# Kernel optimization log

Measured on AMD Instinct MI355X. Metric: run time of the kernel, lower is better.

The kernel has to match this reference:

```python
import jax, jax.numpy as jnp
import numpy as np
import math

# ---- static config (matches init_kwargs) ----
MUL = 16                       # multiplicity of 0e and 1o irreps in/out
IN_DIM = 4 * MUL               # 16x0e + 16x1o -> 16 + 48 = 64 channels
DIAMETER = 7.0
RADIUS = DIAMETER / 2.0
NRB = 8                        # num_radial_basis
STEPS = (1.0, 1.0, 1.0)
N_PATHS = 5                    # 0x0->0, 1x1->0, 0x1->1, 1x0->1, 1x1->1
WEIGHT_NUMEL = N_PATHS * MUL * MUL  # 1280


def _lattice():
    axes = []
    for st in STEPS:
        s = math.floor(RADIUS / st)
        axes.append(np.arange(-s, s + 1.0) * st)
    return np.stack(np.meshgrid(*axes, indexing='ij'), axis=-1).astype(np.float32)  # [kx,ky,kz,3]


def _radial_emb(r):
    # e3nn soft_one_hot_linspace, basis='smooth_finite', cutoff=True
    values = np.linspace(0.0, RADIUS, NRB + 2)[1:-1].astype(np.float32)
    step = values[1] - values[0]
    diff = (r[..., None] - values) / step
    def u(t):  # soft unit step: exp(-1/t) for t>0 else 0
        return np.where(t > 0.0, np.exp(-1.0 / np.where(t > 0.0, t, 1.0)), 0.0)
    return (1.14136 * math.e ** 2 * u(diff + 1.0) * u(1.0 - diff)).astype(np.float32)


def _spherical_harmonics(lat):
    # normalize=True, normalization='component': Y0 = 1, Y1 = sqrt(3) * unit_vec
    n = np.linalg.norm(lat, axis=-1, keepdims=True)
    unit = np.where(n > 0, lat / np.where(n > 0, n, 1.0), 0.0)
    return np.ones(lat.shape[:-1], np.float32), (math.sqrt(3.0) * unit).astype(np.float32)


_LAT = _lattice()
_EMB = jnp.asarray(_radial_emb(np.linalg.norm(_LAT, axis=-1)))  # [kx,ky,kz,NRB]
_sh0_np, _sh1_np = _spherical_harmonics(_LAT)
_SH0, _SH1 = jnp.asarray(_sh0_np), jnp.asarray(_sh1_np)
_eps_np = np.zeros((3, 3, 3), np.float32)
for _i, _j, _k in [(0, 1, 2), (1, 2, 0), (2, 0, 1)]:
    _eps_np[_i, _j, _k] = 1.0
    _eps_np[_i, _k, _j] = -1.0
_EPS = jnp.asarray(_eps_np)


def _build_kernel(tp_weight):
    """Radial-basis matmul + CG tensor-product -> conv kernel [out,in,kx,ky,kz]."""
    kx, ky, kz = _LAT.shape[:3]
    nk = kx * ky * kz
    w = jnp.einsum('xyzb,bn->xyzn', _EMB, tp_weight) / nk
    w = w.reshape(kx, ky, kz, N_PATHS, MUL, MUL)
    w1, w2, w3, w4, w5 = [w[..., p, :, :] for p in range(N_PATHS)]
    # e3nn path weights ('component' norm, 'element' path norm): sqrt(dim_out / fan_in)
    a0 = math.sqrt(1.0 / (2 * MUL))  # -> 0e: paths 1,2 each mul1*mul2 = MUL
    a1 = math.sqrt(3.0 / (3 * MUL))  # -> 1o: paths 3,4,5
    c1 = a0                          # w3j(0,0,0) = 1
    c2 = a0 / math.sqrt(3.0)         # w3j(1,1,0) = delta/sqrt(3)
    c3 = a1 / math.sqrt(3.0)         # w3j(0,1,1) = delta/sqrt(3)
    c4 = a1 / math.sqrt(3.0)         # w3j(1,0,1) = delta/sqrt(3)
    c5 = a1 / math.sqrt(6.0)         # w3j(1,1,1) = eps/sqrt(6)
    Kss = c1 * _SH0[..., None, None] * w1                                  # [k,u,o]
    Kvs = c2 * jnp.einsum('xyzi,xyzuo->xyzuio', _SH1, w2)                  # [k,u,3,o]
    Ksv = c3 * jnp.einsum('xyzk,xyzuo->xyzuok', _SH1, w3)                  # [k,u,o,3]
    eye3 = jnp.eye(3, dtype=w.dtype)
    Kvv = (c4 * jnp.einsum('xyz,ik,xyzuo->xyzuiok', _SH0, eye3, w4)
           + c5 * jnp.einsum('ijk,xyzj,xyzuo->xyzuiok', _EPS, _SH1, w5))   # [k,u,3,o,3]
    top = jnp.concatenate([Kss, Ksv.reshape(kx, ky, kz, MUL, 3 * MUL)], axis=-1)
    bot = jnp.concatenate([Kvs.reshape(kx, ky, kz, 3 * MUL, MUL),
                           Kvv.reshape(kx, ky, kz, 3 * MUL, 3 * MUL)], axis=-1)
    K = jnp.concatenate([top, bot], axis=-2)                               # [kx,ky,kz,in,out]
    return jnp.transpose(K, (4, 3, 0, 1, 2))                               # oixyz


def setup_inputs() -> dict:
    key = jax.random.key(0)
    k1, k2, k3, k4 = jax.random.split(key, 4)
    x = jax.random.normal(k1, (2, IN_DIM, 40, 40, 40), jnp.float32)
    sc_w0 = jax.random.normal(k2, (MUL, MUL), jnp.float32)
    sc_w1 = jax.random.normal(k3, (MUL, MUL), jnp.float32)
    tp_weight = jax.random.normal(k4, (NRB, WEIGHT_NUMEL), jnp.float32)
    return {"x": x, "sc_w0": sc_w0, "sc_w1": sc_w1, "tp_weight": tp_weight}


def reference(x, sc_w0, sc_w1, tp_weight):
    B = x.shape[0]
    sp = x.shape[2:]
    inv = 1.0 / math.sqrt(MUL)  # e3nn Linear fan-in normalization
    x0 = x[:, :MUL]                                  # [B,MUL,D,H,W]
    x1 = x[:, MUL:].reshape(B, MUL, 3, *sp)          # [B,MUL,3,D,H,W]
    sc0 = jnp.einsum('uo,budhw->bodhw', sc_w0, x0) * inv
    sc1 = jnp.einsum('uo,buidhw->boidhw', sc_w1, x1) * inv
    sc = jnp.concatenate([sc0, sc1.reshape(B, 3 * MUL, *sp)], axis=1)
    K = _build_kernel(tp_weight)
    pad = [(s // 2, s // 2) for s in K.shape[2:]]
    conv = jax.lax.conv_general_dilated(
        x, K, window_strides=(1, 1, 1), padding=pad,
        dimension_numbers=('NCDHW', 'OIDHW', 'NCDHW'))
    return sc + conv
```

## Files before the change

kernel.cpp:

```cpp
#include <hip/hip_runtime.h>
#include <stdint.h>


#define NT_REAL 179
#define NT_PAD  180
#define NGRP    45

#define XCH  1557376
#define XCHB ((size_t)XCH * 2)

typedef short s16x8 __attribute__((ext_vector_type(8)));
typedef float f32x4 __attribute__((ext_vector_type(4)));

struct Taps {
  int n;
  short dl16[NT_PAD];
  unsigned char dz[NT_PAD], dy[NT_PAD], dx[NT_PAD];
};
constexpr Taps mk_taps() {
  Taps t{};
  t.n = 0;
  for (int a = 0; a < 7; ++a)
    for (int b = 0; b < 7; ++b)
      for (int c = 0; c < 7; ++c) {
        int d2 = (a-3)*(a-3) + (b-3)*(b-3) + (c-3)*(c-3);
        if (d2 <= 12) {
          t.dz[t.n] = (unsigned char)a; t.dy[t.n] = (unsigned char)b;
          t.dx[t.n] = (unsigned char)c;
          t.dl16[t.n] = (short)((a*14 + b)*16 + c);
          ++t.n;
        }
      }
  for (int i = t.n; i < NT_PAD; ++i) {
    t.dz[i] = 3; t.dy[i] = 3; t.dx[i] = 3; t.dl16[i] = t.dl16[0];
  }
  return t;
}
__device__ constexpr Taps TAPS = mk_taps();
static_assert(mk_taps().n == NT_REAL, "tap count");

struct DL4s { unsigned long long v[NGRP]; };
constexpr DL4s mk_dl4() {
  DL4s d{};
  Taps t = mk_taps();
  for (int g = 0; g < NGRP; ++g) {
    unsigned long long v = 0;
    for (int q = 0; q < 4; ++q)
      v |= (unsigned long long)(unsigned short)t.dl16[g * 4 + q] << (16 * q);
    d.v[g] = v;
  }
  return d;
}
__device__ constexpr DL4s DL4 = mk_dl4();

static __device__ inline unsigned short f2bf(float f) {
  unsigned int u = __float_as_uint(f);
  unsigned int r = u + 0x7FFFu + ((u >> 16) & 1u);
  return (unsigned short)(r >> 16);
}

__device__ __forceinline__ void gl_lds16(const void* g, void* s) {
  __builtin_amdgcn_global_load_lds(
      (const __attribute__((address_space(1))) void*)g,
      (__attribute__((address_space(3))) void*)s, 16, 0, 0);
}

__global__ void prep(const float* __restrict__ x, const float* __restrict__ scw0,
                     const float* __restrict__ scw1, const float* __restrict__ tpw,
                     unsigned short* __restrict__ Xp, unsigned short* __restrict__ Bwp) {
  __shared__ float buf[160 * 65];
  int tid = threadIdx.x;

  if (blockIdx.x < 800) {
    int blk = blockIdx.x;
    int ys = blk % 10; int t2 = blk / 10; int iz = t2 % 40; int b = t2 / 40;
    int y0 = ys * 4;
    const float* src = x + (size_t)b * 4096000 + (size_t)iz * 1600 + (size_t)y0 * 40;
    for (int e = tid; e < 64 * 160; e += 256) {
      int ch = e / 160, i = e - ch * 160;
      buf[i * 65 + ch] = src[(size_t)ch * 64000 + i];
    }
    __syncthreads();
    for (int f = tid; f < 160 * 8; f += 256) {
      int i = f >> 3, g = f & 7;
      int yy = i / 40, xx = i - yy * 40;
      s16x8 v;
      #pragma unroll
      for (int j = 0; j < 8; ++j) v[j] = (short)f2bf(buf[i * 65 + g * 8 + j]);
      size_t pos = ((size_t)((b * 46 + iz + 3) * 46 + (y0 + yy + 3)) * 46 + (xx + 3));
      *reinterpret_cast<s16x8*>(Xp + (size_t)g * XCH + pos * 8) = v;
    }
    return;
  }

  int t = blockIdx.x - 800;
  float (*wsm)[16][16] = reinterpret_cast<float (*)[16][16]>(buf);

  int dz = TAPS.dz[t], dy = TAPS.dy[t], dx = TAPS.dx[t];
  float fz = dz - 3.0f, fy = dy - 3.0f, fx = dx - 3.0f;
  float d2 = fz*fz + fy*fy + fx*fx;
  float r = sqrtf(d2);

  const float step = 3.5f / 9.0f;
  const float Cc = 1.14136f * 7.38905609893065f;
  float emb[8];
  for (int bb = 0; bb < 8; ++bb) {
    float diff = (r - step * (bb + 1)) / step;
    float t1 = diff + 1.0f, t2 = 1.0f - diff;
    float u1 = (t1 > 0.0f) ? expf(-1.0f / t1) : 0.0f;
    float u2 = (t2 > 0.0f) ? expf(-1.0f / t2) : 0.0f;
    emb[bb] = Cc * u1 * u2;
  }

  int u = tid >> 4, o = tid & 15;
  for (int p = 0; p < 5; ++p) {
    float acc = 0.0f;
    int nidx = (p * 16 + u) * 16 + o;
    for (int bb = 0; bb < 8; ++bb) acc += emb[bb] * tpw[bb * 1280 + nidx];
    wsm[p][u][o] = acc * (1.0f / 343.0f);
  }
  __syncthreads();

  float invr = (d2 > 0.0f) ? (1.7320508075688772f / r) : 0.0f;
  float sh[3] = { fz * invr, fy * invr, fx * invr };

  bool center = (dz == 3 && dy == 3 && dx == 3);
  bool padt = (t >= NT_REAL);
  const float c1 = 0.17677669529663687f;
  const float c2 = 0.10206207261596575f;
  const float c3 = 0.14433756729740643f;
  const float c4 = 0.14433756729740643f;
  const float c5 = 0.10206207261596575f;
  const float inv = 0.25f;

  for (int e = tid; e < 4096; e += 256) {
    int ich = e & 63, och = e >> 6;
    float v = 0.0f;
    if (!padt) {
      if (och < 16) {
        if (ich < 16) {
          v = c1 * wsm[0][ich][och];
          if (center) v += inv * scw0[ich * 16 + och];
        } else {
          int qq = ich - 16; int uu = qq / 3, ii = qq % 3;
          v = c2 * sh[ii] * wsm[1][uu][och];
        }
      } else {
        int qo = och - 16; int oo = qo / 3, kk = qo % 3;
        if (ich < 16) {
          v = c3 * sh[kk] * wsm[2][ich][oo];
        } else {
          int qi = ich - 16; int uu = qi / 3, ii = qi % 3;
          if (ii == kk) {
            v = c4 * wsm[3][uu][oo];
            if (center) v += inv * scw1[uu * 16 + oo];
          } else {
            int jj = 3 - ii - kk;
            float sgn = (((kk - ii + 3) % 3) == 2) ? 1.0f : -1.0f;
            v = c5 * sgn * sh[jj] * wsm[4][uu][oo];
          }
        }
      }
    }
    int chunk = ich >> 3, j = ich & 7, q = t & 3, grp = t >> 2;
    int nt = och >> 4, n = och & 15;
    size_t idx = (((((size_t)chunk * NGRP + grp) * 4 + nt) * 4 + q) * 16 + n) * 8 + j;
    Bwp[idx] = f2bf(v);
  }
}

__global__ __launch_bounds__(256, 2) void conv3d(
    const unsigned short* __restrict__ Xp,
    const unsigned short* __restrict__ Bwp,
    float* __restrict__ out) {
  __shared__ __align__(16) unsigned char smem[76800];
  unsigned char* XH = smem;
  unsigned char* BB = smem + 35840;

  int blk = blockIdx.x;
  int p = ((blk & 7) << 6) | (blk >> 3);
  if (p >= 500) return;
  int b = p / 250; int rem = p - b * 250;
  int tz = rem / 25, ty = (rem / 5) % 5, tx = rem % 5;

  int tid = threadIdx.x;
  int lane = tid & 63;
  int w = tid >> 6;
  int q = lane >> 4, n = lane & 15;
  int qs = q << 4;

  size_t hbase = (size_t)(((b * 46 + tz * 4) * 46 + ty * 8) * 46 + tx * 8) * 16;

  int abase = w * 224 + ((n >> 3) << 4) + (n & 7);

  f32x4 acc[4][4];
  #pragma unroll
  for (int a = 0; a < 4; ++a)
    #pragma unroll
    for (int nt = 0; nt < 4; ++nt) acc[a][nt] = f32x4{0.f, 0.f, 0.f, 0.f};

  auto stageB = [&](int c, int s, unsigned char* dst) {
    const unsigned char* bg = (const unsigned char*)Bwp
        + ((size_t)c * NGRP + s * 5) * 4096;
    for (int k = w; k < 20; k += 4)
      gl_lds16(bg + (k << 10) + lane * 16, dst + (k << 10));
  };
  auto stageH = [&](int c) {
    const unsigned char* xc = (const unsigned char*)Xp + (size_t)c * XCHB + hbase;
    for (int k = w; k < 35; k += 4) {
      int sl = (k << 6) + lane;
      int hx = sl & 15; hx = hx > 13 ? 13 : hx;
      int r = sl >> 4;
      int hz = (r * 2341) >> 15;
      int hy = r - hz * 14;
      gl_lds16(xc + ((size_t)((hz * 46 + hy) * 46 + hx)) * 16, XH + (k << 10));
    }
  };

  stageB(0, 0, BB);

  int t = 0;
  for (int c = 0; c < 8; ++c) {
    stageH(c);
    __syncthreads();
    for (int s = 0; s < 9; ++s, ++t) {
      if (t + 1 < 72) {
        int cn = (s == 8) ? c + 1 : c;
        int sn = (s == 8) ? 0 : s + 1;
        stageB(cn, sn, BB + ((t + 1) & 1) * 20480);
      }
      const unsigned char* BSc = BB + (t & 1) * 20480 + (size_t)lane * 16;
      #pragma unroll
      for (int gg = 0; gg < 5; ++gg) {
        unsigned long long dlv = DL4.v[s * 5 + gg];
        int dl = (int)((dlv >> qs) & 0xFFFFull);
        const unsigned char* ab = XH + ((size_t)(abase + dl) << 4);
        s16x8 a0 = *(const s16x8*)(ab);
        s16x8 a1 = *(const s16x8*)(ab + 512);
        s16x8 a2 = *(const s16x8*)(ab + 1024);
        s16x8 a3 = *(const s16x8*)(ab + 1536);
        const unsigned char* bp = BSc + (gg << 12);
        s16x8 b0 = *(const s16x8*)(bp);
        s16x8 b1 = *(const s16x8*)(bp + 1024);
        s16x8 b2 = *(const s16x8*)(bp + 2048);
        s16x8 b3 = *(const s16x8*)(bp + 3072);
        acc[0][0] = __builtin_amdgcn_mfma_f32_16x16x32_bf16(a0, b0, acc[0][0], 0, 0, 0);
        acc[0][1] = __builtin_amdgcn_mfma_f32_16x16x32_bf16(a0, b1, acc[0][1], 0, 0, 0);
        acc[0][2] = __builtin_amdgcn_mfma_f32_16x16x32_bf16(a0, b2, acc[0][2], 0, 0, 0);
        acc[0][3] = __builtin_amdgcn_mfma_f32_16x16x32_bf16(a0, b3, acc[0][3], 0, 0, 0);
        acc[1][0] = __builtin_amdgcn_mfma_f32_16x16x32_bf16(a1, b0, acc[1][0], 0, 0, 0);
        acc[1][1] = __builtin_amdgcn_mfma_f32_16x16x32_bf16(a1, b1, acc[1][1], 0, 0, 0);
        acc[1][2] = __builtin_amdgcn_mfma_f32_16x16x32_bf16(a1, b2, acc[1][2], 0, 0, 0);
        acc[1][3] = __builtin_amdgcn_mfma_f32_16x16x32_bf16(a1, b3, acc[1][3], 0, 0, 0);
        acc[2][0] = __builtin_amdgcn_mfma_f32_16x16x32_bf16(a2, b0, acc[2][0], 0, 0, 0);
        acc[2][1] = __builtin_amdgcn_mfma_f32_16x16x32_bf16(a2, b1, acc[2][1], 0, 0, 0);
        acc[2][2] = __builtin_amdgcn_mfma_f32_16x16x32_bf16(a2, b2, acc[2][2], 0, 0, 0);
        acc[2][3] = __builtin_amdgcn_mfma_f32_16x16x32_bf16(a2, b3, acc[2][3], 0, 0, 0);
        acc[3][0] = __builtin_amdgcn_mfma_f32_16x16x32_bf16(a3, b0, acc[3][0], 0, 0, 0);
        acc[3][1] = __builtin_amdgcn_mfma_f32_16x16x32_bf16(a3, b1, acc[3][1], 0, 0, 0);
        acc[3][2] = __builtin_amdgcn_mfma_f32_16x16x32_bf16(a3, b2, acc[3][2], 0, 0, 0);
        acc[3][3] = __builtin_amdgcn_mfma_f32_16x16x32_bf16(a3, b3, acc[3][3], 0, 0, 0);
      }
      __syncthreads();
    }
  }

  #pragma unroll
  for (int nt = 0; nt < 4; ++nt) {
    size_t cb = (size_t)(b * 64 + nt * 16 + n) * 64000
              + (size_t)(tz * 4 + w) * 1600
              + (size_t)(tx * 8 + (q & 1) * 4);
    #pragma unroll
    for (int a = 0; a < 4; ++a) {
      float* dst = out + cb + (size_t)(ty * 8 + a * 2 + (q >> 1)) * 40;
      *reinterpret_cast<f32x4*>(dst) = acc[a][nt];
    }
  }
}

extern "C" void kernel_launch(void* const* d_in, const int* in_sizes, int n_in,
                              void* d_out, int out_size, void* d_ws, size_t ws_size,
                              hipStream_t stream) {
  const float* x    = (const float*)d_in[0];
  const float* scw0 = (const float*)d_in[1];
  const float* scw1 = (const float*)d_in[2];
  const float* tpw  = (const float*)d_in[3];
  float* out = (float*)d_out;

  unsigned short* Xp  = (unsigned short*)d_ws;
  unsigned short* Bwp = Xp + (size_t)8 * XCH;

  hipMemsetAsync(Xp, 0, (size_t)8 * XCH * 2, stream);
  prep<<<800 + NT_PAD, 256, 0, stream>>>(x, scw0, scw1, tpw, Xp, Bwp);
  conv3d<<<512, 256, 0, stream>>>(Xp, Bwp, out);
}
```

Baseline: 236.3 us.

## Load weights directly to registers and double-buffer input halo in LDS

Weight (B) fragments are no longer staged through shared memory. Each wave now reads them straight from global memory into registers, with a three-deep software pipeline of register buffers. The input halo tile is double-buffered in LDS, and the next channel chunk is prefetched gradually during the middle groups of the current chunk's compute. This cuts the barriers from one per tap-group step to one per channel chunk. In exchange, every wave fetches B redundantly from global/L2, register pressure rises, and global load latency is now exposed inside the MFMA loop.

```diff
diff --git a/kernel.cpp b/kernel.cpp
--- a/kernel.cpp
+++ b/kernel.cpp
@@ -173,9 +173,7 @@
     const unsigned short* __restrict__ Xp,
     const unsigned short* __restrict__ Bwp,
     float* __restrict__ out) {
-  __shared__ __align__(16) unsigned char smem[76800];
-  unsigned char* XH = smem;
-  unsigned char* BB = smem + 35840;
+  __shared__ __align__(16) unsigned char smem[71680];
 
   int blk = blockIdx.x;
   int p = ((blk & 7) << 6) | (blk >> 3);
@@ -199,70 +197,76 @@
     #pragma unroll
     for (int nt = 0; nt < 4; ++nt) acc[a][nt] = f32x4{0.f, 0.f, 0.f, 0.f};
 
-  auto stageB = [&](int c, int s, unsigned char* dst) {
-    const unsigned char* bg = (const unsigned char*)Bwp
-        + ((size_t)c * NGRP + s * 5) * 4096;
-    for (int k = w; k < 20; k += 4)
-      gl_lds16(bg + (k << 10) + lane * 16, dst + (k << 10));
+  auto stageH1 = [&](int c, unsigned char* dst, int k) {
+    const unsigned char* xc = (const unsigned char*)Xp + (size_t)c * XCHB + hbase;
+    int sl = (k << 6) + lane;
+    int hx = sl & 15; hx = hx > 13 ? 13 : hx;
+    int r = sl >> 4;
+    int hz = (r * 2341) >> 15;
+    int hy = r - hz * 14;
+    gl_lds16(xc + ((size_t)((hz * 46 + hy) * 46 + hx)) * 16, dst + (k << 10));
   };
-  auto stageH = [&](int c) {
-    const unsigned char* xc = (const unsigned char*)Xp + (size_t)c * XCHB + hbase;
-    for (int k = w; k < 35; k += 4) {
-      int sl = (k << 6) + lane;
-      int hx = sl & 15; hx = hx > 13 ? 13 : hx;
-      int r = sl >> 4;
-      int hz = (r * 2341) >> 15;
-      int hy = r - hz * 14;
-      gl_lds16(xc + ((size_t)((hz * 46 + hy) * 46 + hx)) * 16, XH + (k << 10));
-    }
-  };
-
-  stageB(0, 0, BB);
-
-  int t = 0;
+
+  for (int k = w; k < 35; k += 4) stageH1(0, smem, k);
+  __syncthreads();
+
   for (int c = 0; c < 8; ++c) {
-    stageH(c);
+    const unsigned char* XHc = smem + (c & 1) * 35840;
+    unsigned char* XHn = smem + ((c + 1) & 1) * 35840;
+
+    const unsigned char* bgc = (const unsigned char*)Bwp
+        + (size_t)c * (NGRP * 4096) + (size_t)lane * 16;
+
+    s16x8 bf0[4], bf1[4], bf2[4];
+    auto loadB = [&](s16x8* dst, int g) {
+      const s16x8* pp = (const s16x8*)(bgc + (size_t)g * 4096);
+      dst[0] = pp[0]; dst[1] = pp[64]; dst[2] = pp[128]; dst[3] = pp[192];
+    };
+    auto compute = [&](int g, const s16x8* bfr) {
+      unsigned long long dlv = DL4.v[g];
+      int dl = (int)((dlv >> qs) & 0xFFFFull);
+      const unsigned char* ab = XHc + ((size_t)(abase + dl) << 4);
+      s16x8 a0 = *(const s16x8*)(ab);
+      s16x8 a1 = *(const s16x8*)(ab + 512);
+      s16x8 a2 = *(const s16x8*)(ab + 1024);
+      s16x8 a3 = *(const s16x8*)(ab + 1536);
+      acc[0][0] = __builtin_amdgcn_mfma_f32_16x16x32_bf16(a0, bfr[0], acc[0][0], 0, 0, 0);
+      acc[0][1] = __builtin_amdgcn_mfma_f32_16x16x32_bf16(a0, bfr[1], acc[0][1], 0, 0, 0);
+      acc[0][2] = __builtin_amdgcn_mfma_f32_16x16x32_bf16(a0, bfr[2], acc[0][2], 0, 0, 0);
+      acc[0][3] = __builtin_amdgcn_mfma_f32_16x16x32_bf16(a0, bfr[3], acc[0][3], 0, 0, 0);
+      acc[1][0] = __builtin_amdgcn_mfma_f32_16x16x32_bf16(a1, bfr[0], acc[1][0], 0, 0, 0);
+      acc[1][1] = __builtin_amdgcn_mfma_f32_16x16x32_bf16(a1, bfr[1], acc[1][1], 0, 0, 0);
+      acc[1][2] = __builtin_amdgcn_mfma_f32_16x16x32_bf16(a1, bfr[2], acc[1][2], 0, 0, 0);
+      acc[1][3] = __builtin_amdgcn_mfma_f32_16x16x32_bf16(a1, bfr[3], acc[1][3], 0, 0, 0);
+      acc[2][0] = __builtin_amdgcn_mfma_f32_16x16x32_bf16(a2, bfr[0], acc[2][0], 0, 0, 0);
+      acc[2][1] = __builtin_amdgcn_mfma_f32_16x16x32_bf16(a2, bfr[1], acc[2][1], 0, 0, 0);
+      acc[2][2] = __builtin_amdgcn_mfma_f32_16x16x32_bf16(a2, bfr[2], acc[2][2], 0, 0, 0);
+      acc[2][3] = __builtin_amdgcn_mfma_f32_16x16x32_bf16(a2, bfr[3], acc[2][3], 0, 0, 0);
+      acc[3][0] = __builtin_amdgcn_mfma_f32_16x16x32_bf16(a3, bfr[0], acc[3][0], 0, 0, 0);
+      acc[3][1] = __builtin_amdgcn_mfma_f32_16x16x32_bf16(a3, bfr[1], acc[3][1], 0, 0, 0);
+      acc[3][2] = __builtin_amdgcn_mfma_f32_16x16x32_bf16(a3, bfr[2], acc[3][2], 0, 0, 0);
+      acc[3][3] = __builtin_amdgcn_mfma_f32_16x16x32_bf16(a3, bfr[3], acc[3][3], 0, 0, 0);
+    };
+
+    loadB(bf0, 0);
+    loadB(bf1, 1);
+    #pragma unroll 1
+    for (int g = 0; g < NGRP; g += 3) {
+      if (c < 7 && g >= 12 && g <= 36) {
+        int k = ((g - 12) / 3) * 4 + w;
+        if (k < 35) stageH1(c + 1, XHn, k);
+      }
+      int g2 = g + 2 < NGRP ? g + 2 : NGRP - 1;
+      int g3 = g + 3 < NGRP ? g + 3 : NGRP - 1;
+      int g4 = g + 4 < NGRP ? g + 4 : NGRP - 1;
+      loadB(bf2, g2);
+      compute(g, bf0);
+      loadB(bf0, g3);
+      compute(g + 1, bf1);
+      loadB(bf1, g4);
+      compute(g + 2, bf2);
+    }
     __syncthreads();
-    for (int s = 0; s < 9; ++s, ++t) {
-      if (t + 1 < 72) {
-        int cn = (s == 8) ? c + 1 : c;
-        int sn = (s == 8) ? 0 : s + 1;
-        stageB(cn, sn, BB + ((t + 1) & 1) * 20480);
-      }
-      const unsigned char* BSc = BB + (t & 1) * 20480 + (size_t)lane * 16;
-      #pragma unroll
-      for (int gg = 0; gg < 5; ++gg) {
-        unsigned long long dlv = DL4.v[s * 5 + gg];
-        int dl = (int)((dlv >> qs) & 0xFFFFull);
-        const unsigned char* ab = XH + ((size_t)(abase + dl) << 4);
-        s16x8 a0 = *(const s16x8*)(ab);
-        s16x8 a1 = *(const s16x8*)(ab + 512);
-        s16x8 a2 = *(const s16x8*)(ab + 1024);
-        s16x8 a3 = *(const s16x8*)(ab + 1536);
-        const unsigned char* bp = BSc + (gg << 12);
-        s16x8 b0 = *(const s16x8*)(bp);
-        s16x8 b1 = *(const s16x8*)(bp + 1024);
-        s16x8 b2 = *(const s16x8*)(bp + 2048);
-        s16x8 b3 = *(const s16x8*)(bp + 3072);
-        acc[0][0] = __builtin_amdgcn_mfma_f32_16x16x32_bf16(a0, b0, acc[0][0], 0, 0, 0);
-        acc[0][1] = __builtin_amdgcn_mfma_f32_16x16x32_bf16(a0, b1, acc[0][1], 0, 0, 0);
-        acc[0][2] = __builtin_amdgcn_mfma_f32_16x16x32_bf16(a0, b2, acc[0][2], 0, 0, 0);
-        acc[0][3] = __builtin_amdgcn_mfma_f32_16x16x32_bf16(a0, b3, acc[0][3], 0, 0, 0);
-        acc[1][0] = __builtin_amdgcn_mfma_f32_16x16x32_bf16(a1, b0, acc[1][0], 0, 0, 0);
-        acc[1][1] = __builtin_amdgcn_mfma_f32_16x16x32_bf16(a1, b1, acc[1][1], 0, 0, 0);
-        acc[1][2] = __builtin_amdgcn_mfma_f32_16x16x32_bf16(a1, b2, acc[1][2], 0, 0, 0);
-        acc[1][3] = __builtin_amdgcn_mfma_f32_16x16x32_bf16(a1, b3, acc[1][3], 0, 0, 0);
-        acc[2][0] = __builtin_amdgcn_mfma_f32_16x16x32_bf16(a2, b0, acc[2][0], 0, 0, 0);
-        acc[2][1] = __builtin_amdgcn_mfma_f32_16x16x32_bf16(a2, b1, acc[2][1], 0, 0, 0);
-        acc[2][2] = __builtin_amdgcn_mfma_f32_16x16x32_bf16(a2, b2, acc[2][2], 0, 0, 0);
-        acc[2][3] = __builtin_amdgcn_mfma_f32_16x16x32_bf16(a2, b3, acc[2][3], 0, 0, 0);
-        acc[3][0] = __builtin_amdgcn_mfma_f32_16x16x32_bf16(a3, b0, acc[3][0], 0, 0, 0);
-        acc[3][1] = __builtin_amdgcn_mfma_f32_16x16x32_bf16(a3, b1, acc[3][1], 0, 0, 0);
-        acc[3][2] = __builtin_amdgcn_mfma_f32_16x16x32_bf16(a3, b2, acc[3][2], 0, 0, 0);
-        acc[3][3] = __builtin_amdgcn_mfma_f32_16x16x32_bf16(a3, b3, acc[3][3], 0, 0, 0);
-      }
-      __syncthreads();
-    }
   }
 
   #pragma unroll
```

After: 243.3 us. +3.0%, slower.
